# Kernel tuning notes

Hardware: AMD Instinct MI355X
Metric: run time of the kernel (lower is better)

Reference implementation:

```python
import jax, jax.numpy as jnp
import numpy as np

C = 64        # in_channels
E = 64        # embed_dim
K_RATIO = 0.5


def _conv(x, w, b, pad, groups):
    # x: [B,C,H,W], w: [O, I/groups, kh, kw] (torch OIHW layout)
    y = jax.lax.conv_general_dilated(
        x, w, window_strides=(1, 1), padding=[(pad, pad), (pad, pad)],
        dimension_numbers=("NCHW", "OIHW", "NCHW"), feature_group_count=groups)
    return y + b[None, :, None, None]


def setup_inputs() -> dict:
    key = jax.random.key(0)
    ks = jax.random.split(key, 16)
    s = 0.05
    return {
        "x": jax.random.normal(ks[0], (8, C, 64, 64), jnp.float32),
        "w1": jax.random.normal(ks[1], (C, C, 1, 1), jnp.float32) * s,
        "b1": jax.random.normal(ks[2], (C,), jnp.float32) * s,
        "w3": jax.random.normal(ks[3], (C, 1, 3, 3), jnp.float32) * s,
        "b3": jax.random.normal(ks[4], (C,), jnp.float32) * s,
        "w5": jax.random.normal(ks[5], (C, 1, 5, 5), jnp.float32) * s,
        "b5": jax.random.normal(ks[6], (C,), jnp.float32) * s,
        "qw": jax.random.normal(ks[7], (E, 3 * C), jnp.float32) * s,
        "qb": jax.random.normal(ks[8], (E,), jnp.float32) * s,
        "kw": jax.random.normal(ks[9], (E, 3 * C), jnp.float32) * s,
        "kb": jax.random.normal(ks[10], (E,), jnp.float32) * s,
        "vw": jax.random.normal(ks[11], (C, 3 * C), jnp.float32) * s,
        "vb": jax.random.normal(ks[12], (C,), jnp.float32) * s,
        "ow": jax.random.normal(ks[13], (C, C), jnp.float32) * s,
        "ob": jax.random.normal(ks[14], (C,), jnp.float32) * s,
    }


def reference(x, w1, b1, w3, b3, w5, b5, qw, qb, kw, kb, vw, vb, ow, ob):
    b, c, h, w = x.shape
    N = h * w
    f1 = _conv(x, w1, b1, pad=0, groups=1)        # 1x1 conv
    f2 = _conv(x, w3, b3, pad=1, groups=c)        # 3x3 depthwise
    f3 = _conv(x, w5, b5, pad=2, groups=c)        # 5x5 depthwise
    f_multi = jnp.concatenate([f1, f2, f3], axis=1)           # [b, 3c, h, w]
    f_flat = f_multi.reshape(b, 3 * c, N).transpose(0, 2, 1)  # [b, N, 3c]

    Q = jnp.einsum("bnd,ed->bne", f_flat, qw) + qb            # [b, N, E]
    K = jnp.einsum("bnd,ed->bne", f_flat, kw) + kb            # [b, N, E]
    V = jnp.einsum("bnd,cd->bnc", f_flat, vw) + vb            # [b, N, c]

    attn = jnp.einsum("bqe,bke->bqk", Q, K) / jnp.sqrt(jnp.float32(E))
    attn = jax.nn.softmax(attn, axis=-1)                      # [b, N, N]

    key_importance = attn.sum(axis=1)                         # [b, N]
    k_val = max(1, min(int(N * K_RATIO), N))
    _, topk_idx = jax.lax.top_k(key_importance, k_val)        # [b, k_val]
    mask = jnp.zeros_like(key_importance).at[
        jnp.arange(b)[:, None], topk_idx].set(1.0)            # [b, N]

    attn_c = attn * mask[:, None, :]
    attn_c = attn_c / (attn_c.sum(axis=-1, keepdims=True) + 1e-8)
    out = jnp.einsum("bqk,bkc->bqc", attn_c, V)               # [b, N, c]
    out = jnp.einsum("bnc,oc->bno", out, ow) + ob
    return out.transpose(0, 2, 1).reshape(b, c, h, w)
```

## Files before the change

### kernel.cpp

```cpp
#include <hip/hip_runtime.h>
#include <hip/hip_bf16.h>

typedef unsigned short ushort;
typedef __bf16 bf16x8 __attribute__((ext_vector_type(8)));
typedef float f32x4 __attribute__((ext_vector_type(4)));

__device__ __forceinline__ ushort f2bu(float f) {
  __hip_bfloat16 h = __float2bfloat16(f);
  return *(ushort*)&h;
}
__device__ __forceinline__ float bu2f(ushort u) {
  unsigned int v = ((unsigned int)u) << 16;
  return __uint_as_float(v);
}
__device__ __forceinline__ f32x4 mfma16(bf16x8 a, bf16x8 b, f32x4 c) {
  return __builtin_amdgcn_mfma_f32_16x16x32_bf16(a, b, c, 0, 0, 0);
}
__device__ __forceinline__ float fexp2(float x) { return __builtin_amdgcn_exp2f(x); }


__global__ __launch_bounds__(256) void k_conv(
    const float* __restrict__ x, const float* __restrict__ w1t, const float* __restrict__ b1,
    const float* __restrict__ w3, const float* __restrict__ b3,
    const float* __restrict__ w5, const float* __restrict__ b5,
    ushort* __restrict__ f) {
  __shared__ ushort Xs[5 * 64 * 74];
  const int tid = threadIdx.x;
  const int y = blockIdx.x;
  const int b = blockIdx.y;
  for (int i = tid; i < 320 * 5; i += 256) {
    int r = i / 5, pp = i % 5;
    int col = (pp < 2) ? 2 * pp : 68 + 2 * (pp - 2);
    *(unsigned int*)&Xs[r * 74 + col] = 0u;
  }
#pragma unroll
  for (int k = 0; k < 20; k++) {
    int idx = tid + k * 256;
    int px4 = idx & 15, ch = (idx >> 4) & 63, yy = idx >> 10;
    int ysrc = y + yy - 2;
    float4 v = make_float4(0.f, 0.f, 0.f, 0.f);
    if (ysrc >= 0 && ysrc < 64)
      v = *(const float4*)&x[(((size_t)(b * 64 + ch) * 64) + ysrc) * 64 + px4 * 4];
    unsigned int lo = (unsigned int)f2bu(v.x) | ((unsigned int)f2bu(v.y) << 16);
    unsigned int hi = (unsigned int)f2bu(v.z) | ((unsigned int)f2bu(v.w) << 16);
    int base = (yy * 64 + ch) * 74 + 4 + px4 * 4;
    *(unsigned int*)&Xs[base] = lo;
    *(unsigned int*)&Xs[base + 2] = hi;
  }
  __syncthreads();
  const int px = tid & 63;
  const int cbu = __builtin_amdgcn_readfirstlane((tid >> 6) * 16);
  ushort* fo = f + ((size_t)b * 4096 + y * 64 + px) * 192;
  float a1[16];
#pragma unroll
  for (int j = 0; j < 16; j++) a1[j] = b1[cbu + j];
  for (int ic = 0; ic < 64; ic++) {
    float xv = bu2f(Xs[(2 * 64 + ic) * 74 + 4 + px]);
    const float* wrow = &w1t[ic * 64 + cbu];
#pragma unroll
    for (int j = 0; j < 16; j++) a1[j] += wrow[j] * xv;
  }
#pragma unroll
  for (int j = 0; j < 16; j++) fo[cbu + j] = f2bu(a1[j]);
#pragma unroll 4
  for (int j = 0; j < 16; j++) {
    int c = cbu + j;
    float a3 = b3[c], a5 = b5[c];
#pragma unroll
    for (int dy = 0; dy < 5; dy++) {
      const ushort* row = &Xs[(dy * 64 + c) * 74 + 2 + px];
#pragma unroll
      for (int dx = 0; dx < 5; dx++) {
        float v = bu2f(row[dx]);
        a5 += w5[c * 25 + dy * 5 + dx] * v;
        if (dy >= 1 && dy <= 3 && dx >= 1 && dx <= 3)
          a3 += w3[c * 9 + (dy - 1) * 3 + (dx - 1)] * v;
      }
    }
    fo[64 + c] = f2bu(a3);
    fo[128 + c] = f2bu(a5);
  }
}

__global__ __launch_bounds__(256) void k_w2b(
    const float* __restrict__ qw, const float* __restrict__ kw,
    const float* __restrict__ vw, const float* __restrict__ w1,
    ushort* __restrict__ Wb, float* __restrict__ w1t) {
  int i = blockIdx.x * 256 + threadIdx.x;
  if (i < 36864) {
    const float* src = (i < 12288) ? qw : (i < 24576) ? kw : vw;
    int off = (i < 12288) ? i : (i < 24576) ? (i - 12288) : (i - 24576);
    Wb[i] = f2bu(src[off]);
  } else {
    int j = i - 36864;
    if (j < 4096) w1t[(j & 63) * 64 + (j >> 6)] = w1[j];
  }
}

__global__ __launch_bounds__(256) void k_qkv(
    const ushort* __restrict__ F, const ushort* __restrict__ Wb,
    const float* __restrict__ qb, const float* __restrict__ kb,
    const float* __restrict__ vb,
    ushort* __restrict__ Q, ushort* __restrict__ K, ushort* __restrict__ V) {
  __shared__ __align__(16) ushort fs[64][200];
  const int tid = threadIdx.x;
  const int w = tid >> 6;
  const int lane = tid & 63;
  const int col = lane & 15;
  const int quad = lane >> 4;
  const size_t rowbase = (size_t)blockIdx.x * 64;
  for (int i = tid; i < 1536; i += 256) {
    int r = i / 24, c8 = i % 24;
    *(uint4*)&fs[r][c8 * 8] = *(const uint4*)&F[rowbase * 192 + (size_t)i * 8];
  }
  __syncthreads();
  bf16x8 af[6];
#pragma unroll
  for (int kk = 0; kk < 6; kk++)
    af[kk] = *(const bf16x8*)&fs[w * 16 + col][kk * 32 + quad * 8];
  ushort* const outp[3] = {Q, K, V};
  const float* const bp[3] = {qb, kb, vb};
#pragma unroll
  for (int sel = 0; sel < 3; sel++) {
    const ushort* wsel = Wb + sel * 12288;
    const float sc = (sel == 0) ? 0.125f * 1.44269504088896f : 1.0f;
#pragma unroll
    for (int ntl = 0; ntl < 4; ntl++) {
      const ushort* brow = wsel + (ntl * 16 + col) * 192 + quad * 8;
      f32x4 acc = {0.f, 0.f, 0.f, 0.f};
#pragma unroll
      for (int kk = 0; kk < 6; kk++) {
        bf16x8 bf = *(const bf16x8*)&brow[kk * 32];
        acc = mfma16(af[kk], bf, acc);
      }
      float bv = bp[sel][ntl * 16 + col];
#pragma unroll
      for (int r = 0; r < 4; r++)
        outp[sel][(rowbase + w * 16 + quad * 4 + r) * 64 + ntl * 16 + col] =
            f2bu((acc[r] + bv) * sc);
    }
  }
}

__global__ __launch_bounds__(256) void k_sumexp_l(
    const ushort* __restrict__ Qb, const ushort* __restrict__ Kb,
    float* __restrict__ Lp) {
  __shared__ float red[4][64];
  const int tid = threadIdx.x;
  const int b = blockIdx.x & 7;
  const int rest = blockIdx.x >> 3;
  const int qt = rest & 63;
  const int kh = rest >> 6;
  const int lane = tid & 63;
  const int w = tid >> 6;
  const int col = lane & 15;
  const int quad = lane >> 4;
  const size_t qbase = (size_t)b * 4096 + qt * 64;
  const size_t kbase = (size_t)b * 4096 + kh * 2048;
  bf16x8 af[4][2];
#pragma unroll
  for (int t = 0; t < 4; t++)
#pragma unroll
    for (int h = 0; h < 2; h++)
      af[t][h] = *(const bf16x8*)&Qb[(qbase + t * 16 + col) * 64 + quad * 8 + h * 32];
  const ushort* kp = &Kb[(kbase + w * 16 + col) * 64 + quad * 8];
  float lacc[4][4];
#pragma unroll
  for (int t = 0; t < 4; t++)
#pragma unroll
    for (int r = 0; r < 4; r++) lacc[t][r] = 0.f;
  bf16x8 nb0 = *(const bf16x8*)kp;
  bf16x8 nb1 = *(const bf16x8*)(kp + 32);
#pragma unroll 1
  for (int kt = 0; kt < 32; kt++) {
    bf16x8 b0 = nb0, b1 = nb1;
    if (kt < 31) {
      nb0 = *(const bf16x8*)(kp + (size_t)(kt + 1) * 4096);
      nb1 = *(const bf16x8*)(kp + (size_t)(kt + 1) * 4096 + 32);
    }
#pragma unroll
    for (int t = 0; t < 4; t++) {
      f32x4 acc = {0.f, 0.f, 0.f, 0.f};
      acc = mfma16(af[t][0], b0, acc);
      acc = mfma16(af[t][1], b1, acc);
#pragma unroll
      for (int r = 0; r < 4; r++) lacc[t][r] += fexp2(acc[r]);
    }
  }
#pragma unroll
  for (int t = 0; t < 4; t++)
#pragma unroll
    for (int r = 0; r < 4; r++) {
      float v = lacc[t][r];
      v += __shfl_xor(v, 1); v += __shfl_xor(v, 2);
      v += __shfl_xor(v, 4); v += __shfl_xor(v, 8);
      if (col == 0) red[w][t * 16 + quad * 4 + r] = v;
    }
  __syncthreads();
  if (tid < 64) {
    float l = red[0][tid] + red[1][tid] + red[2][tid] + red[3][tid];
    Lp[((size_t)(b * 64 + qt) * 2 + kh) * 64 + tid] = l;
  }
}

__global__ __launch_bounds__(256) void k_lcomb(
    const float* __restrict__ Lp, float* __restrict__ Lo, float* __restrict__ Linv) {
  int i = blockIdx.x * 256 + threadIdx.x;
  int bqt = i >> 6, q = i & 63;
  float l = Lp[(size_t)bqt * 128 + q] + Lp[(size_t)bqt * 128 + 64 + q];
  Lo[i] = l;
  Linv[i] = 1.f / l;
}

__global__ __launch_bounds__(256) void k_sumexp_ip(
    const ushort* __restrict__ Qb, const ushort* __restrict__ Kb,
    const float* __restrict__ Linv, float* __restrict__ IP) {
  __shared__ float lred[64];
  const int tid = threadIdx.x;
  const int b = blockIdx.x & 7;
  const int rest = blockIdx.x >> 3;
  const int qt = rest & 63;
  const int kh = rest >> 6;
  const int lane = tid & 63;
  const int w = tid >> 6;
  const int col = lane & 15;
  const int quad = lane >> 4;
  const size_t qbase = (size_t)b * 4096 + qt * 64;
  const size_t kbase = (size_t)b * 4096 + kh * 2048;
  if (tid < 64) lred[tid] = Linv[qbase + tid];
  bf16x8 af[4][2];
#pragma unroll
  for (int t = 0; t < 4; t++)
#pragma unroll
    for (int h = 0; h < 2; h++)
      af[t][h] = *(const bf16x8*)&Qb[(qbase + t * 16 + col) * 64 + quad * 8 + h * 32];
  __syncthreads();
  float linv[4][4];
#pragma unroll
  for (int t = 0; t < 4; t++)
#pragma unroll
    for (int r = 0; r < 4; r++) linv[t][r] = lred[t * 16 + quad * 4 + r];
  const ushort* kp = &Kb[(kbase + w * 16 + col) * 64 + quad * 8];
  bf16x8 nb0 = *(const bf16x8*)kp;
  bf16x8 nb1 = *(const bf16x8*)(kp + 32);
#pragma unroll 1
  for (int kt = 0; kt < 32; kt++) {
    bf16x8 b0 = nb0, b1 = nb1;
    if (kt < 31) {
      nb0 = *(const bf16x8*)(kp + (size_t)(kt + 1) * 4096);
      nb1 = *(const bf16x8*)(kp + (size_t)(kt + 1) * 4096 + 32);
    }
    float ip = 0.f;
#pragma unroll
    for (int t = 0; t < 4; t++) {
      f32x4 acc = {0.f, 0.f, 0.f, 0.f};
      acc = mfma16(af[t][0], b0, acc);
      acc = mfma16(af[t][1], b1, acc);
#pragma unroll
      for (int r = 0; r < 4; r++) ip += fexp2(acc[r]) * linv[t][r];
    }
    ip += __shfl_xor(ip, 16);
    ip += __shfl_xor(ip, 32);
    if (quad == 0)
      IP[((size_t)(b * 64 + qt)) * 4096 + (kh * 32 + kt) * 64 + w * 16 + col] = ip;
  }
}

__global__ __launch_bounds__(256) void k_impsum(
    const float* __restrict__ IP, float* __restrict__ imp) {
  const int tid = threadIdx.x;
  const int b = blockIdx.y;
  const int col = blockIdx.x * 256 + tid;
  const float* p = IP + (size_t)b * 64 * 4096 + col;
  float s = 0.f;
#pragma unroll 8
  for (int r = 0; r < 64; r++) s += p[(size_t)r * 4096];
  imp[(size_t)b * 4096 + col] = s;
}

__global__ __launch_bounds__(256) void k_mask2c(
    const float* __restrict__ imp, const ushort* __restrict__ Kb,
    const ushort* __restrict__ Vb, ushort* __restrict__ Kc,
    ushort* __restrict__ Vc) {
  __shared__ __align__(16) float imps[4096];
  __shared__ int part[4][64];
  const int tid = threadIdx.x;
  const int b = blockIdx.y;
  const int base = blockIdx.x * 64;
  for (int i = tid; i < 4096; i += 256) imps[i] = imp[(size_t)b * 4096 + i];
  __syncthreads();
  const int cand = tid & 63;
  const int seg = tid >> 6;
  const int k = base + cand;
  const float v = imps[k];
  int cnt = 0;
  const int j0 = seg * 1024;
  for (int j = j0; j < j0 + 1024; j += 4) {
    float4 a = *(const float4*)&imps[j];
    cnt += (a.x > v) ? 1 : ((a.x == v && (j + 0) < k) ? 1 : 0);
    cnt += (a.y > v) ? 1 : ((a.y == v && (j + 1) < k) ? 1 : 0);
    cnt += (a.z > v) ? 1 : ((a.z == v && (j + 2) < k) ? 1 : 0);
    cnt += (a.w > v) ? 1 : ((a.w == v && (j + 3) < k) ? 1 : 0);
  }
  part[seg][cand] = cnt;
  __syncthreads();
  const int c = part[0][cand] + part[1][cand] + part[2][cand] + part[3][cand];
  if (c < 2048) {
    const ushort* ksrc = &Kb[((size_t)b * 4096 + k) * 64 + seg * 16];
    const ushort* vsrc = &Vb[((size_t)b * 4096 + k) * 64 + seg * 16];
    ushort* kdst = &Kc[((size_t)b * 2048 + c) * 64 + seg * 16];
    ushort* vdst = &Vc[((size_t)b * 2048 + c) * 64 + seg * 16];
    *(uint4*)kdst = *(const uint4*)ksrc;
    *(uint4*)(kdst + 8) = *(const uint4*)(ksrc + 8);
    *(uint4*)vdst = *(const uint4*)vsrc;
    *(uint4*)(vdst + 8) = *(const uint4*)(vsrc + 8);
  }
}

__global__ __launch_bounds__(256) void k_attn_out(
    const ushort* __restrict__ Qb, const ushort* __restrict__ Kc,
    const ushort* __restrict__ Vc, const float* __restrict__ Lo,
    const float* __restrict__ owp, const float* __restrict__ obp,
    float* __restrict__ out) {
  __shared__ __align__(16) ushort Vt[64][72];
  __shared__ __align__(16) ushort Ps[64][72];
  __shared__ __align__(16) ushort ows[64][72];
  __shared__ float dred[4][64];
  __shared__ float lqs[64];
  const int tid = threadIdx.x;
  const int b = blockIdx.x & 7;
  const int qt = blockIdx.x >> 3;
  const int lane = tid & 63;
  const int w = tid >> 6;
  const int col = lane & 15;
  const int quad = lane >> 4;
  const size_t qbase = (size_t)b * 4096 + qt * 64;
  const size_t kbase = (size_t)b * 2048;
  bf16x8 af[4][2];
#pragma unroll
  for (int t = 0; t < 4; t++)
#pragma unroll
    for (int h = 0; h < 2; h++)
      af[t][h] = *(const bf16x8*)&Qb[(qbase + t * 16 + col) * 64 + quad * 8 + h * 32];
  for (int i = tid; i < 4096; i += 256) ows[i >> 6][i & 63] = f2bu(owp[i]);
  if (tid < 64) lqs[tid] = Lo[qbase + tid];
  f32x4 pv[4];
  float dpacc[4][4];
#pragma unroll
  for (int t = 0; t < 4; t++) {
    pv[t] = (f32x4){0.f, 0.f, 0.f, 0.f};
#pragma unroll
    for (int r = 0; r < 4; r++) dpacc[t][r] = 0.f;
  }
  const int vrow = tid & 63;
  const int vch = tid >> 6;
  const ushort* kp = &Kc[(kbase + w * 16 + col) * 64 + quad * 8];
  bf16x8 nb0 = *(const bf16x8*)kp;
  bf16x8 nb1 = *(const bf16x8*)(kp + 32);
  for (int kt = 0; kt < 32; kt++) {
    __syncthreads();
    {
      const ushort* vsrc = &Vc[(kbase + kt * 64 + vrow) * 64 + vch * 16];
      uint4 v0 = *(const uint4*)vsrc;
      uint4 v1 = *(const uint4*)(vsrc + 8);
      ushort tmp[16];
      *(uint4*)&tmp[0] = v0;
      *(uint4*)&tmp[8] = v1;
#pragma unroll
      for (int j = 0; j < 16; j++) Vt[vch * 16 + j][vrow] = tmp[j];
    }
    bf16x8 b0 = nb0, b1 = nb1;
    if (kt < 31) {
      nb0 = *(const bf16x8*)(kp + (size_t)(kt + 1) * 4096);
      nb1 = *(const bf16x8*)(kp + (size_t)(kt + 1) * 4096 + 32);
    }
#pragma unroll
    for (int t = 0; t < 4; t++) {
      f32x4 acc = {0.f, 0.f, 0.f, 0.f};
      acc = mfma16(af[t][0], b0, acc);
      acc = mfma16(af[t][1], b1, acc);
#pragma unroll
      for (int r = 0; r < 4; r++) {
        float p = fexp2(acc[r]);
        dpacc[t][r] += p;
        Ps[t * 16 + quad * 4 + r][w * 16 + col] = f2bu(p);
      }
    }
    __syncthreads();
    bf16x8 v0f = *(const bf16x8*)&Vt[w * 16 + col][quad * 8];
    bf16x8 v1f = *(const bf16x8*)&Vt[w * 16 + col][quad * 8 + 32];
#pragma unroll
    for (int t = 0; t < 4; t++) {
      bf16x8 p0 = *(const bf16x8*)&Ps[t * 16 + col][quad * 8];
      bf16x8 p1 = *(const bf16x8*)&Ps[t * 16 + col][quad * 8 + 32];
      pv[t] = mfma16(p0, v0f, pv[t]);
      pv[t] = mfma16(p1, v1f, pv[t]);
    }
  }
#pragma unroll
  for (int t = 0; t < 4; t++)
#pragma unroll
    for (int r = 0; r < 4; r++) {
      float v = dpacc[t][r];
      v += __shfl_xor(v, 1); v += __shfl_xor(v, 2);
      v += __shfl_xor(v, 4); v += __shfl_xor(v, 8);
      if (col == 0) dred[w][t * 16 + quad * 4 + r] = v;
    }
  __syncthreads();
#pragma unroll
  for (int t = 0; t < 4; t++)
#pragma unroll
    for (int r = 0; r < 4; r++) {
      int q = t * 16 + quad * 4 + r;
      float den = dred[0][q] + dred[1][q] + dred[2][q] + dred[3][q] + 1e-8f * lqs[q];
      Ps[q][w * 16 + col] = f2bu(pv[t][r] / den);
    }
  __syncthreads();
  bf16x8 w0 = *(const bf16x8*)&ows[w * 16 + col][quad * 8];
  bf16x8 w1 = *(const bf16x8*)&ows[w * 16 + col][quad * 8 + 32];
  const float obv = obp[w * 16 + col];
#pragma unroll
  for (int t = 0; t < 4; t++) {
    bf16x8 p0 = *(const bf16x8*)&Ps[t * 16 + col][quad * 8];
    bf16x8 p1 = *(const bf16x8*)&Ps[t * 16 + col][quad * 8 + 32];
    f32x4 oc = {0.f, 0.f, 0.f, 0.f};
    oc = mfma16(p0, w0, oc);
    oc = mfma16(p1, w1, oc);
#pragma unroll
    for (int r = 0; r < 4; r++) {
      int q = t * 16 + quad * 4 + r;
      int co = w * 16 + col;
      out[((size_t)(b * 64 + co)) * 4096 + qt * 64 + q] = oc[r] + obv;
    }
  }
}

extern "C" void kernel_launch(void* const* d_in, const int* in_sizes, int n_in,
                              void* d_out, int out_size, void* d_ws, size_t ws_size,
                              hipStream_t stream) {
  const float* x  = (const float*)d_in[0];
  const float* w1 = (const float*)d_in[1];
  const float* b1 = (const float*)d_in[2];
  const float* w3 = (const float*)d_in[3];
  const float* b3 = (const float*)d_in[4];
  const float* w5 = (const float*)d_in[5];
  const float* b5 = (const float*)d_in[6];
  const float* qw = (const float*)d_in[7];
  const float* qb = (const float*)d_in[8];
  const float* kw = (const float*)d_in[9];
  const float* kb = (const float*)d_in[10];
  const float* vw = (const float*)d_in[11];
  const float* vb = (const float*)d_in[12];
  const float* ow = (const float*)d_in[13];
  const float* ob = (const float*)d_in[14];
  float* out = (float*)d_out;
  float* ws = (float*)d_ws;
  ushort* F    = (ushort*)ws;
  ushort* Qb   = (ushort*)(ws + 3145728);
  ushort* Kb   = (ushort*)(ws + 4194304);
  ushort* Vb   = (ushort*)(ws + 5242880);
  float*  Lo   = ws + 6291456;
  float*  Linv = ws + 6324224;
  float*  Lp   = ws + 6356992;
  float*  IP   = ws + 6422528;
  float*  imp  = ws + 8519680;
  ushort* Kc   = (ushort*)(ws + 8552448);
  ushort* Vc   = (ushort*)(ws + 9076736);
  ushort* Wb   = (ushort*)(ws + 9601024);
  float*  w1t  = ws + 9619456;

  k_w2b<<<160, 256, 0, stream>>>(qw, kw, vw, w1, Wb, w1t);
  k_conv<<<dim3(64, 8), 256, 0, stream>>>(x, w1t, b1, w3, b3, w5, b5, F);
  k_qkv<<<512, 256, 0, stream>>>(F, Wb, qb, kb, vb, Qb, Kb, Vb);
  k_sumexp_l<<<1024, 256, 0, stream>>>(Qb, Kb, Lp);
  k_lcomb<<<128, 256, 0, stream>>>(Lp, Lo, Linv);
  k_sumexp_ip<<<1024, 256, 0, stream>>>(Qb, Kb, Linv, IP);
  k_impsum<<<dim3(16, 8), 256, 0, stream>>>(IP, imp);
  k_mask2c<<<dim3(64, 8), 256, 0, stream>>>(imp, Kb, Vb, Kc, Vc);
  k_attn_out<<<512, 256, 0, stream>>>(Qb, Kc, Vc, Lo, ow, ob, out);
}
```

Before: 306.4 us.

## Split attention-output over key halves and fold L-combine into consumers

Removes the k_lcomb kernel by computing the inverse row sum inline in k_sumexp_ip and the combine kernel. Splits the final attention kernel into two key halves (1024 blocks instead of 512) that write unnormalized projected partial outputs and denominators. A new combine kernel sums the halves, normalizes, adds bias, and transposes to NCHW. This is meant to raise parallelism in the last stage, at the cost of an extra kernel and roughly 16MB of fp32 partial-output traffic.

```diff
diff --git a/kernel.cpp b/kernel.cpp
--- a/kernel.cpp
+++ b/kernel.cpp
@@ -203,18 +203,9 @@
   }
 }
 
-__global__ __launch_bounds__(256) void k_lcomb(
-    const float* __restrict__ Lp, float* __restrict__ Lo, float* __restrict__ Linv) {
-  int i = blockIdx.x * 256 + threadIdx.x;
-  int bqt = i >> 6, q = i & 63;
-  float l = Lp[(size_t)bqt * 128 + q] + Lp[(size_t)bqt * 128 + 64 + q];
-  Lo[i] = l;
-  Linv[i] = 1.f / l;
-}
-
 __global__ __launch_bounds__(256) void k_sumexp_ip(
     const ushort* __restrict__ Qb, const ushort* __restrict__ Kb,
-    const float* __restrict__ Linv, float* __restrict__ IP) {
+    const float* __restrict__ Lp, float* __restrict__ IP) {
   __shared__ float lred[64];
   const int tid = threadIdx.x;
   const int b = blockIdx.x & 7;
@@ -227,7 +218,9 @@
   const int quad = lane >> 4;
   const size_t qbase = (size_t)b * 4096 + qt * 64;
   const size_t kbase = (size_t)b * 4096 + kh * 2048;
-  if (tid < 64) lred[tid] = Linv[qbase + tid];
+  const size_t bqt = (size_t)(b * 64 + qt);
+  if (tid < 64)
+    lred[tid] = 1.f / (Lp[bqt * 128 + tid] + Lp[bqt * 128 + 64 + tid]);
   bf16x8 af[4][2];
 #pragma unroll
   for (int t = 0; t < 4; t++)
@@ -317,25 +310,26 @@
   }
 }
 
-__global__ __launch_bounds__(256) void k_attn_out(
+__global__ __launch_bounds__(256) void k_attn_po(
     const ushort* __restrict__ Qb, const ushort* __restrict__ Kc,
-    const ushort* __restrict__ Vc, const float* __restrict__ Lo,
-    const float* __restrict__ owp, const float* __restrict__ obp,
-    float* __restrict__ out) {
+    const ushort* __restrict__ Vc, const float* __restrict__ owp,
+    float* __restrict__ OPp, float* __restrict__ Dp) {
   __shared__ __align__(16) ushort Vt[64][72];
   __shared__ __align__(16) ushort Ps[64][72];
   __shared__ __align__(16) ushort ows[64][72];
   __shared__ float dred[4][64];
-  __shared__ float lqs[64];
   const int tid = threadIdx.x;
   const int b = blockIdx.x & 7;
-  const int qt = blockIdx.x >> 3;
+  const int rest = blockIdx.x >> 3;
+  const int qt = rest & 63;
+  const int kh = rest >> 6;
   const int lane = tid & 63;
   const int w = tid >> 6;
   const int col = lane & 15;
   const int quad = lane >> 4;
   const size_t qbase = (size_t)b * 4096 + qt * 64;
-  const size_t kbase = (size_t)b * 2048;
+  const size_t kbase = (size_t)b * 2048 + kh * 1024;
+  const size_t bidx = (size_t)(b * 64 + qt) * 2 + kh;
   bf16x8 af[4][2];
 #pragma unroll
   for (int t = 0; t < 4; t++)
@@ -343,7 +337,6 @@
     for (int h = 0; h < 2; h++)
       af[t][h] = *(const bf16x8*)&Qb[(qbase + t * 16 + col) * 64 + quad * 8 + h * 32];
   for (int i = tid; i < 4096; i += 256) ows[i >> 6][i & 63] = f2bu(owp[i]);
-  if (tid < 64) lqs[tid] = Lo[qbase + tid];
   f32x4 pv[4];
   float dpacc[4][4];
 #pragma unroll
@@ -357,7 +350,8 @@
   const ushort* kp = &Kc[(kbase + w * 16 + col) * 64 + quad * 8];
   bf16x8 nb0 = *(const bf16x8*)kp;
   bf16x8 nb1 = *(const bf16x8*)(kp + 32);
-  for (int kt = 0; kt < 32; kt++) {
+#pragma unroll 1
+  for (int kt = 0; kt < 16; kt++) {
     __syncthreads();
     {
       const ushort* vsrc = &Vc[(kbase + kt * 64 + vrow) * 64 + vch * 16];
@@ -370,7 +364,7 @@
       for (int j = 0; j < 16; j++) Vt[vch * 16 + j][vrow] = tmp[j];
     }
     bf16x8 b0 = nb0, b1 = nb1;
-    if (kt < 31) {
+    if (kt < 15) {
       nb0 = *(const bf16x8*)(kp + (size_t)(kt + 1) * 4096);
       nb1 = *(const bf16x8*)(kp + (size_t)(kt + 1) * 4096 + 32);
     }
@@ -407,18 +401,16 @@
       if (col == 0) dred[w][t * 16 + quad * 4 + r] = v;
     }
   __syncthreads();
-#pragma unroll
-  for (int t = 0; t < 4; t++)
-#pragma unroll
-    for (int r = 0; r < 4; r++) {
-      int q = t * 16 + quad * 4 + r;
-      float den = dred[0][q] + dred[1][q] + dred[2][q] + dred[3][q] + 1e-8f * lqs[q];
-      Ps[q][w * 16 + col] = f2bu(pv[t][r] / den);
-    }
+  if (tid < 64)
+    Dp[bidx * 64 + tid] = dred[0][tid] + dred[1][tid] + dred[2][tid] + dred[3][tid];
+#pragma unroll
+  for (int t = 0; t < 4; t++)
+#pragma unroll
+    for (int r = 0; r < 4; r++)
+      Ps[t * 16 + quad * 4 + r][w * 16 + col] = f2bu(pv[t][r]);
   __syncthreads();
   bf16x8 w0 = *(const bf16x8*)&ows[w * 16 + col][quad * 8];
   bf16x8 w1 = *(const bf16x8*)&ows[w * 16 + col][quad * 8 + 32];
-  const float obv = obp[w * 16 + col];
 #pragma unroll
   for (int t = 0; t < 4; t++) {
     bf16x8 p0 = *(const bf16x8*)&Ps[t * 16 + col][quad * 8];
@@ -430,8 +422,39 @@
     for (int r = 0; r < 4; r++) {
       int q = t * 16 + quad * 4 + r;
       int co = w * 16 + col;
-      out[((size_t)(b * 64 + co)) * 4096 + qt * 64 + q] = oc[r] + obv;
-    }
+      OPp[bidx * 4096 + q * 64 + co] = oc[r];
+    }
+  }
+}
+
+__global__ __launch_bounds__(256) void k_attn_comb(
+    const float* __restrict__ OPp, const float* __restrict__ Dp,
+    const float* __restrict__ Lp, const float* __restrict__ obp,
+    float* __restrict__ out) {
+  __shared__ float T[64 * 65];
+  __shared__ float rden[64];
+  __shared__ float obs[64];
+  const int tid = threadIdx.x;
+  const int b = blockIdx.x & 7;
+  const int qt = blockIdx.x >> 3;
+  const size_t bqt = (size_t)(b * 64 + qt);
+  if (tid < 64) {
+    float d = Dp[bqt * 128 + tid] + Dp[bqt * 128 + 64 + tid];
+    float l = Lp[bqt * 128 + tid] + Lp[bqt * 128 + 64 + tid];
+    rden[tid] = 1.f / (d + 1e-8f * l);
+    obs[tid] = obp[tid];
+  }
+  __syncthreads();
+  const float* A = OPp + bqt * 2 * 4096;
+  const float* Bh = A + 4096;
+  for (int i = tid; i < 4096; i += 256) {
+    int q = i >> 6, co = i & 63;
+    T[co * 65 + q] = (A[i] + Bh[i]) * rden[q];
+  }
+  __syncthreads();
+  for (int i = tid; i < 4096; i += 256) {
+    int co = i >> 6, q = i & 63;
+    out[((size_t)(b * 64 + co)) * 4096 + qt * 64 + q] = T[co * 65 + q] + obs[co];
   }
 }
 
@@ -459,23 +482,23 @@
   ushort* Qb   = (ushort*)(ws + 3145728);
   ushort* Kb   = (ushort*)(ws + 4194304);
   ushort* Vb   = (ushort*)(ws + 5242880);
-  float*  Lo   = ws + 6291456;
-  float*  Linv = ws + 6324224;
-  float*  Lp   = ws + 6356992;
-  float*  IP   = ws + 6422528;
-  float*  imp  = ws + 8519680;
-  ushort* Kc   = (ushort*)(ws + 8552448);
-  ushort* Vc   = (ushort*)(ws + 9076736);
-  ushort* Wb   = (ushort*)(ws + 9601024);
-  float*  w1t  = ws + 9619456;
+  float*  Lp   = ws + 6291456;
+  float*  IP   = ws + 6356992;
+  float*  imp  = ws + 8454144;
+  ushort* Kc   = (ushort*)(ws + 8486912);
+  ushort* Vc   = (ushort*)(ws + 9011200);
+  ushort* Wb   = (ushort*)(ws + 9535488);
+  float*  w1t  = ws + 9553920;
+  float*  OPp  = ws + 9558016;
+  float*  Dp   = ws + 13752320;
 
   k_w2b<<<160, 256, 0, stream>>>(qw, kw, vw, w1, Wb, w1t);
   k_conv<<<dim3(64, 8), 256, 0, stream>>>(x, w1t, b1, w3, b3, w5, b5, F);
   k_qkv<<<512, 256, 0, stream>>>(F, Wb, qb, kb, vb, Qb, Kb, Vb);
   k_sumexp_l<<<1024, 256, 0, stream>>>(Qb, Kb, Lp);
-  k_lcomb<<<128, 256, 0, stream>>>(Lp, Lo, Linv);
-  k_sumexp_ip<<<1024, 256, 0, stream>>>(Qb, Kb, Linv, IP);
+  k_sumexp_ip<<<1024, 256, 0, stream>>>(Qb, Kb, Lp, IP);
   k_impsum<<<dim3(16, 8), 256, 0, stream>>>(IP, imp);
   k_mask2c<<<dim3(64, 8), 256, 0, stream>>>(imp, Kb, Vb, Kc, Vc);
-  k_attn_out<<<512, 256, 0, stream>>>(Qb, Kc, Vc, Lo, ow, ob, out);
-}
+  k_attn_po<<<1024, 256, 0, stream>>>(Qb, Kc, Vc, ow, OPp, Dp);
+  k_attn_comb<<<512, 256, 0, stream>>>(OPp, Dp, Lp, ob, out);
+}
```

New measurement: 304.3 us. Within noise of the previous version (-0.7%).
